# Optimization experiments

Hardware: AMD Instinct MI355X
Metric: run time of the kernel (lower is better)

The kernel has to match this reference:

```python
import jax, jax.numpy as jnp
import numpy as np

B, H, S, D = 4, 16, 2048, 128

def setup_inputs() -> dict:
    key = jax.random.key(0)
    k1, k2 = jax.random.split(key)
    x2 = jax.random.normal(k1, (B, H, S, D), dtype=jnp.float32)
    x3 = jax.random.normal(k2, (B, H, S, D), dtype=jnp.float32)
    return {"x2": x2, "x3": x3}

def reference(x2, x3):
    # scores: [B,H,S,S] = x2 @ x3^T (unscaled)
    scores = jnp.einsum('bhqd,bhkd->bhqk', x2, x3)
    probs = jax.nn.softmax(scores, axis=-1)
    # output: [B,H,S,D] = probs @ x3
    return jnp.einsum('bhqk,bhkd->bhqd', probs, x3)
```

## Files before the change

### kernel.cpp

```cpp
#include <hip/hip_runtime.h>
#include <hip/hip_bf16.h>

typedef __attribute__((ext_vector_type(4))) float f32x4;
typedef _Float16 f16;
typedef __attribute__((ext_vector_type(8))) _Float16 f16x8;
typedef __attribute__((ext_vector_type(2))) __fp16 pk16x2;
typedef __attribute__((ext_vector_type(2))) unsigned int uint2v;

#define S_LEN 2048
#define D_DIM 128
#define QBLK 128
#define KVBLK 64
#define NKV (S_LEN / KVBLK)
#define LOG2E 1.44269504088896340736f
#define EXP2(x) __builtin_amdgcn_exp2f(x)

__device__ __forceinline__ unsigned cvtpk(float a, float b) {
    union { pk16x2 p; unsigned u; } v;
    v.p = __builtin_amdgcn_cvt_pkrtz(a, b);
    return v.u;
}

__device__ __forceinline__ float hired_max(float x) {
    uint2v s = __builtin_amdgcn_permlane16_swap(__float_as_uint(x), __float_as_uint(x), false, false);
    float m = fmaxf(__uint_as_float(s.x), __uint_as_float(s.y));
    uint2v s2 = __builtin_amdgcn_permlane32_swap(__float_as_uint(m), __float_as_uint(m), false, false);
    return fmaxf(__uint_as_float(s2.x), __uint_as_float(s2.y));
}
__device__ __forceinline__ float hired_sum(float x) {
    uint2v s = __builtin_amdgcn_permlane16_swap(__float_as_uint(x), __float_as_uint(x), false, false);
    float m = __uint_as_float(s.x) + __uint_as_float(s.y);
    uint2v s2 = __builtin_amdgcn_permlane32_swap(__float_as_uint(m), __float_as_uint(m), false, false);
    return __uint_as_float(s2.x) + __uint_as_float(s2.y);
}

__global__ __launch_bounds__(256, 2) void attn_kernel(
    const float* __restrict__ Q, const float* __restrict__ KV,
    float* __restrict__ Out)
{
    unsigned b = blockIdx.x;
    unsigned cpx = gridDim.x >> 3;
    unsigned work = (b & 7u) * cpx + (b >> 3);
    unsigned head = work >> 4;
    unsigned qt = work & 15u;

    const float* Qh = Q + (size_t)head * (S_LEN * D_DIM) + (size_t)qt * QBLK * D_DIM;
    const float* Kh = KV + (size_t)head * (S_LEN * D_DIM);
    float* Oh = Out + (size_t)head * (S_LEN * D_DIM) + (size_t)qt * QBLK * D_DIM;

    const int tid = threadIdx.x;
    const int wv = tid >> 6;
    const int lane = tid & 63;
    const int lo = lane & 15;
    const int hi = lane >> 4;

    __shared__ __align__(16) f16 Ksh[KVBLK * D_DIM];
    __shared__ __align__(16) f16 Vsh[D_DIM * KVBLK];

    const int srow = (tid >> 5) * 8;
    const int scol = (tid & 31) * 4;

    f16x8 qf[2][4];
    #pragma unroll
    for (int t = 0; t < 2; ++t) {
        const float* qr = Qh + (wv * 32 + t * 16 + lo) * D_DIM + hi * 8;
        #pragma unroll
        for (int kc = 0; kc < 4; ++kc) {
            f32x4 a = *(const f32x4*)(qr + kc * 32);
            f32x4 c = *(const f32x4*)(qr + kc * 32 + 4);
            union { unsigned u[4]; f16x8 v; } q;
            q.u[0] = cvtpk(a[0] * LOG2E, a[1] * LOG2E);
            q.u[1] = cvtpk(a[2] * LOG2E, a[3] * LOG2E);
            q.u[2] = cvtpk(c[0] * LOG2E, c[1] * LOG2E);
            q.u[3] = cvtpk(c[2] * LOG2E, c[3] * LOG2E);
            qf[t][kc] = q.v;
        }
    }

    f32x4 oacc[2][8];
    #pragma unroll
    for (int t = 0; t < 2; ++t)
        #pragma unroll
        for (int n = 0; n < 8; ++n) oacc[t][n] = (f32x4){0.f, 0.f, 0.f, 0.f};
    float mr[2] = {-1e30f, -1e30f};
    float lr[2] = {0.f, 0.f};

    f32x4 stg[8];
    uint2v kw[8];
    unsigned vw[4][4];

    #define STAGE_LOAD(KT) do {                                               \
        const float* p_ = Kh + (size_t)(KT) * KVBLK * D_DIM + (size_t)srow * D_DIM + scol; \
        _Pragma("unroll")                                                     \
        for (int i_ = 0; i_ < 8; ++i_) stg[i_] = *(const f32x4*)(p_ + i_ * D_DIM); \
    } while (0)

    #define STAGE_PACK() do {                                                 \
        _Pragma("unroll")                                                     \
        for (int i_ = 0; i_ < 8; ++i_) {                                      \
            kw[i_].x = cvtpk(stg[i_][0], stg[i_][1]);                         \
            kw[i_].y = cvtpk(stg[i_][2], stg[i_][3]);                         \
        }                                                                     \
        _Pragma("unroll")                                                     \
        for (int j_ = 0; j_ < 4; ++j_) {                                      \
            vw[j_][0] = cvtpk(stg[0][j_], stg[1][j_]);                        \
            vw[j_][1] = cvtpk(stg[2][j_], stg[3][j_]);                        \
            vw[j_][2] = cvtpk(stg[4][j_], stg[5][j_]);                        \
            vw[j_][3] = cvtpk(stg[6][j_], stg[7][j_]);                        \
        }                                                                     \
    } while (0)

    #define STAGE_WRITE() do {                                                \
        _Pragma("unroll")                                                     \
        for (int i_ = 0; i_ < 8; ++i_) {                                      \
            int row_ = srow + i_;                                             \
            int fK_ = (row_ & 7) ^ ((row_ >> 3) & 7);                         \
            *(uint2v*)&Ksh[row_ * D_DIM + (scol ^ (fK_ << 3))] = kw[i_];      \
        }                                                                     \
        _Pragma("unroll")                                                     \
        for (int j_ = 0; j_ < 4; ++j_) {                                      \
            int d_ = scol + j_;                                               \
            int g_ = (d_ & 7) ^ ((d_ >> 3) & 7);                              \
            union { unsigned u[4]; f16x8 v; } w_;                             \
            w_.u[0] = vw[j_][0]; w_.u[1] = vw[j_][1];                         \
            w_.u[2] = vw[j_][2]; w_.u[3] = vw[j_][3];                         \
            *(f16x8*)&Vsh[d_ * KVBLK + (srow ^ (g_ << 3))] = w_.v;            \
        }                                                                     \
    } while (0)

    STAGE_LOAD(0);
    STAGE_PACK();
    STAGE_WRITE();
    __syncthreads();

    for (int kt = 0; kt < NKV; ++kt) {
        if (kt + 1 < NKV) STAGE_LOAD(kt + 1);

        f32x4 st[2][4];
        #pragma unroll
        for (int t = 0; t < 2; ++t)
            #pragma unroll
            for (int m = 0; m < 4; ++m) st[t][m] = (f32x4){0.f, 0.f, 0.f, 0.f};
        __builtin_amdgcn_s_setprio(1);
        #pragma unroll
        for (int m = 0; m < 4; ++m) {
            int row = m * 16 + lo;
            int fK = (row & 7) ^ ((row >> 3) & 7);
            #pragma unroll
            for (int kc = 0; kc < 4; ++kc) {
                f16x8 kf = *(const f16x8*)&Ksh[row * D_DIM + ((kc * 32 + hi * 8) ^ (fK << 3))];
                st[0][m] = __builtin_amdgcn_mfma_f32_16x16x32_f16(kf, qf[0][kc], st[0][m], 0, 0, 0);
                st[1][m] = __builtin_amdgcn_mfma_f32_16x16x32_f16(kf, qf[1][kc], st[1][m], 0, 0, 0);
            }
        }
        __builtin_amdgcn_s_setprio(0);

        f16x8 pf[2][2];
        #pragma unroll
        for (int t = 0; t < 2; ++t) {
            float mm[4];
            #pragma unroll
            for (int m = 0; m < 4; ++m)
                mm[m] = fmaxf(fmaxf(st[t][m][0], st[t][m][1]),
                              fmaxf(st[t][m][2], st[t][m][3]));
            float tmax = fmaxf(fmaxf(mm[0], mm[1]), fmaxf(mm[2], mm[3]));
            tmax = hired_max(tmax);

            bool skip = __all(tmax - mr[t] <= 11.5415603f);
            float mnew = skip ? mr[t] : fmaxf(mr[t], tmax);

            float sm[4];
            #pragma unroll
            for (int m = 0; m < 4; ++m) {
                float p0 = EXP2(st[t][m][0] - mnew);
                float p1 = EXP2(st[t][m][1] - mnew);
                float p2 = EXP2(st[t][m][2] - mnew);
                float p3 = EXP2(st[t][m][3] - mnew);
                st[t][m][0] = p0; st[t][m][1] = p1;
                st[t][m][2] = p2; st[t][m][3] = p3;
                sm[m] = (p0 + p1) + (p2 + p3);
            }
            float ls = (sm[0] + sm[1]) + (sm[2] + sm[3]);
            ls = hired_sum(ls);

            if (!skip) {
                float scale = EXP2(mr[t] - mnew);
                lr[t] = lr[t] * scale + ls;
                float sc4[4];
                #pragma unroll
                for (int r = 0; r < 4; ++r) sc4[r] = __shfl(scale, hi * 4 + r, 64);
                #pragma unroll
                for (int n = 0; n < 8; ++n)
                    #pragma unroll
                    for (int r = 0; r < 4; ++r) oacc[t][n][r] *= sc4[r];
                mr[t] = mnew;
            } else {
                lr[t] += ls;
            }

            unsigned cc[4][2];
            #pragma unroll
            for (int m = 0; m < 4; ++m) {
                cc[m][0] = cvtpk(st[t][m][0], st[t][m][1]);
                cc[m][1] = cvtpk(st[t][m][2], st[t][m][3]);
            }
            #pragma unroll
            for (int kc2 = 0; kc2 < 2; ++kc2) {
                unsigned r0 = cc[2 * kc2][0], r1 = cc[2 * kc2][1];
                unsigned r2 = cc[2 * kc2 + 1][0], r3 = cc[2 * kc2 + 1][1];
                uint2v s02 = __builtin_amdgcn_permlane32_swap(r0, r2, false, false);
                uint2v s13 = __builtin_amdgcn_permlane32_swap(r1, r3, false, false);
                uint2v t02 = __builtin_amdgcn_permlane16_swap(s02.x, s02.y, false, false);
                uint2v t13 = __builtin_amdgcn_permlane16_swap(s13.x, s13.y, false, false);
                union { unsigned u[4]; f16x8 v; } pu;
                pu.u[0] = t02.x; pu.u[1] = t13.x; pu.u[2] = t02.y; pu.u[3] = t13.y;
                pf[t][kc2] = pu.v;
            }
        }

        __builtin_amdgcn_s_setprio(1);
        #pragma unroll
        for (int kc2 = 0; kc2 < 2; ++kc2) {
            #pragma unroll
            for (int n = 0; n < 8; ++n) {
                int d = n * 16 + lo;
                int g = (d & 7) ^ ((d >> 3) & 7);
                f16x8 vf = *(const f16x8*)&Vsh[d * KVBLK + ((kc2 * 32 + hi * 8) ^ (g << 3))];
                oacc[0][n] = __builtin_amdgcn_mfma_f32_16x16x32_f16(pf[0][kc2], vf, oacc[0][n], 0, 0, 0);
                oacc[1][n] = __builtin_amdgcn_mfma_f32_16x16x32_f16(pf[1][kc2], vf, oacc[1][n], 0, 0, 0);
            }
        }
        __builtin_amdgcn_s_setprio(0);

        if (kt + 1 < NKV) STAGE_PACK();

        __syncthreads();
        if (kt + 1 < NKV) {
            STAGE_WRITE();
            __syncthreads();
        }
    }

    #pragma unroll
    for (int t = 0; t < 2; ++t) {
        float inv = 1.0f / lr[t];
        float rl[4];
        #pragma unroll
        for (int r = 0; r < 4; ++r) rl[r] = __shfl(inv, hi * 4 + r, 64);
        #pragma unroll
        for (int n = 0; n < 8; ++n)
            #pragma unroll
            for (int r = 0; r < 4; ++r)
                Oh[(wv * 32 + t * 16 + hi * 4 + r) * D_DIM + n * 16 + lo] = oacc[t][n][r] * rl[r];
    }
}

extern "C" void kernel_launch(void* const* d_in, const int* in_sizes, int n_in,
                              void* d_out, int out_size, void* d_ws, size_t ws_size,
                              hipStream_t stream) {
    const float* x2 = (const float*)d_in[0];
    const float* x3 = (const float*)d_in[1];
    float* out = (float*)d_out;
    dim3 grid(1024), block(256);
    hipLaunchKernelGGL(attn_kernel, grid, block, 0, stream, x2, x3, out);
}
```

Baseline: 170.6 us.

## Compute softmax row sums via MFMA with ones and fuse staging conversion

The softmax denominator is now accumulated by extra MFMA instructions that multiply the fp16 probability fragments by a ones vector. This replaces the per-tile VALU additions and cross-lane permlane sum reduction. The accumulator lands in the output layout, so the final per-row shuffle of the inverse is dropped. The separate pack stage is removed and fp32-to-fp16 conversion is folded into the LDS write after the barrier, which frees registers but moves conversion work onto the critical path. The max reduction is also rewritten as a flatter fmax tree, and row sums now come from fp16-rounded probabilities.

```diff
diff --git a/kernel.cpp b/kernel.cpp
--- a/kernel.cpp
+++ b/kernel.cpp
@@ -26,12 +26,6 @@
     float m = fmaxf(__uint_as_float(s.x), __uint_as_float(s.y));
     uint2v s2 = __builtin_amdgcn_permlane32_swap(__float_as_uint(m), __float_as_uint(m), false, false);
     return fmaxf(__uint_as_float(s2.x), __uint_as_float(s2.y));
-}
-__device__ __forceinline__ float hired_sum(float x) {
-    uint2v s = __builtin_amdgcn_permlane16_swap(__float_as_uint(x), __float_as_uint(x), false, false);
-    float m = __uint_as_float(s.x) + __uint_as_float(s.y);
-    uint2v s2 = __builtin_amdgcn_permlane32_swap(__float_as_uint(m), __float_as_uint(m), false, false);
-    return __uint_as_float(s2.x) + __uint_as_float(s2.y);
 }
 
 __global__ __launch_bounds__(256, 2) void attn_kernel(
@@ -60,6 +54,11 @@
     const int srow = (tid >> 5) * 8;
     const int scol = (tid & 31) * 4;
 
+    union { unsigned u[4]; f16x8 v; } onesu;
+    onesu.u[0] = 0x3C003C00u; onesu.u[1] = 0x3C003C00u;
+    onesu.u[2] = 0x3C003C00u; onesu.u[3] = 0x3C003C00u;
+    const f16x8 onesf = onesu.v;
+
     f16x8 qf[2][4];
     #pragma unroll
     for (int t = 0; t < 2; ++t) {
@@ -78,16 +77,16 @@
     }
 
     f32x4 oacc[2][8];
+    f32x4 lacc[2];
     #pragma unroll
-    for (int t = 0; t < 2; ++t)
+    for (int t = 0; t < 2; ++t) {
         #pragma unroll
         for (int n = 0; n < 8; ++n) oacc[t][n] = (f32x4){0.f, 0.f, 0.f, 0.f};
+        lacc[t] = (f32x4){0.f, 0.f, 0.f, 0.f};
+    }
     float mr[2] = {-1e30f, -1e30f};
-    float lr[2] = {0.f, 0.f};
 
     f32x4 stg[8];
-    uint2v kw[8];
-    unsigned vw[4][4];
 
     #define STAGE_LOAD(KT) do {                                               \
         const float* p_ = Kh + (size_t)(KT) * KVBLK * D_DIM + (size_t)srow * D_DIM + scol; \
@@ -95,41 +94,30 @@
         for (int i_ = 0; i_ < 8; ++i_) stg[i_] = *(const f32x4*)(p_ + i_ * D_DIM); \
     } while (0)
 
-    #define STAGE_PACK() do {                                                 \
-        _Pragma("unroll")                                                     \
-        for (int i_ = 0; i_ < 8; ++i_) {                                      \
-            kw[i_].x = cvtpk(stg[i_][0], stg[i_][1]);                         \
-            kw[i_].y = cvtpk(stg[i_][2], stg[i_][3]);                         \
-        }                                                                     \
-        _Pragma("unroll")                                                     \
-        for (int j_ = 0; j_ < 4; ++j_) {                                      \
-            vw[j_][0] = cvtpk(stg[0][j_], stg[1][j_]);                        \
-            vw[j_][1] = cvtpk(stg[2][j_], stg[3][j_]);                        \
-            vw[j_][2] = cvtpk(stg[4][j_], stg[5][j_]);                        \
-            vw[j_][3] = cvtpk(stg[6][j_], stg[7][j_]);                        \
-        }                                                                     \
-    } while (0)
-
     #define STAGE_WRITE() do {                                                \
         _Pragma("unroll")                                                     \
         for (int i_ = 0; i_ < 8; ++i_) {                                      \
             int row_ = srow + i_;                                             \
             int fK_ = (row_ & 7) ^ ((row_ >> 3) & 7);                         \
-            *(uint2v*)&Ksh[row_ * D_DIM + (scol ^ (fK_ << 3))] = kw[i_];      \
+            uint2v w_;                                                        \
+            w_.x = cvtpk(stg[i_][0], stg[i_][1]);                             \
+            w_.y = cvtpk(stg[i_][2], stg[i_][3]);                             \
+            *(uint2v*)&Ksh[row_ * D_DIM + (scol ^ (fK_ << 3))] = w_;          \
         }                                                                     \
         _Pragma("unroll")                                                     \
         for (int j_ = 0; j_ < 4; ++j_) {                                      \
             int d_ = scol + j_;                                               \
             int g_ = (d_ & 7) ^ ((d_ >> 3) & 7);                              \
             union { unsigned u[4]; f16x8 v; } w_;                             \
-            w_.u[0] = vw[j_][0]; w_.u[1] = vw[j_][1];                         \
-            w_.u[2] = vw[j_][2]; w_.u[3] = vw[j_][3];                         \
+            w_.u[0] = cvtpk(stg[0][j_], stg[1][j_]);                          \
+            w_.u[1] = cvtpk(stg[2][j_], stg[3][j_]);                          \
+            w_.u[2] = cvtpk(stg[4][j_], stg[5][j_]);                          \
+            w_.u[3] = cvtpk(stg[6][j_], stg[7][j_]);                          \
             *(f16x8*)&Vsh[d_ * KVBLK + (srow ^ (g_ << 3))] = w_.v;            \
         }                                                                     \
     } while (0)
 
     STAGE_LOAD(0);
-    STAGE_PACK();
     STAGE_WRITE();
     __syncthreads();
 
@@ -158,34 +146,28 @@
         f16x8 pf[2][2];
         #pragma unroll
         for (int t = 0; t < 2; ++t) {
-            float mm[4];
-            #pragma unroll
-            for (int m = 0; m < 4; ++m)
-                mm[m] = fmaxf(fmaxf(st[t][m][0], st[t][m][1]),
-                              fmaxf(st[t][m][2], st[t][m][3]));
-            float tmax = fmaxf(fmaxf(mm[0], mm[1]), fmaxf(mm[2], mm[3]));
-            tmax = hired_max(tmax);
+            float a0 = fmaxf(fmaxf(st[t][0][0], st[t][0][1]), st[t][0][2]);
+            float a1 = fmaxf(fmaxf(st[t][0][3], st[t][1][0]), st[t][1][1]);
+            float a2 = fmaxf(fmaxf(st[t][1][2], st[t][1][3]), st[t][2][0]);
+            float a3 = fmaxf(fmaxf(st[t][2][1], st[t][2][2]), st[t][2][3]);
+            float a4 = fmaxf(fmaxf(st[t][3][0], st[t][3][1]), st[t][3][2]);
+            float b0 = fmaxf(fmaxf(a0, a1), a2);
+            float b1 = fmaxf(fmaxf(a3, a4), st[t][3][3]);
+            float tmax = hired_max(fmaxf(b0, b1));
 
             bool skip = __all(tmax - mr[t] <= 11.5415603f);
             float mnew = skip ? mr[t] : fmaxf(mr[t], tmax);
 
-            float sm[4];
             #pragma unroll
             for (int m = 0; m < 4; ++m) {
-                float p0 = EXP2(st[t][m][0] - mnew);
-                float p1 = EXP2(st[t][m][1] - mnew);
-                float p2 = EXP2(st[t][m][2] - mnew);
-                float p3 = EXP2(st[t][m][3] - mnew);
-                st[t][m][0] = p0; st[t][m][1] = p1;
-                st[t][m][2] = p2; st[t][m][3] = p3;
-                sm[m] = (p0 + p1) + (p2 + p3);
-            }
-            float ls = (sm[0] + sm[1]) + (sm[2] + sm[3]);
-            ls = hired_sum(ls);
+                st[t][m][0] = EXP2(st[t][m][0] - mnew);
+                st[t][m][1] = EXP2(st[t][m][1] - mnew);
+                st[t][m][2] = EXP2(st[t][m][2] - mnew);
+                st[t][m][3] = EXP2(st[t][m][3] - mnew);
+            }
 
             if (!skip) {
                 float scale = EXP2(mr[t] - mnew);
-                lr[t] = lr[t] * scale + ls;
                 float sc4[4];
                 #pragma unroll
                 for (int r = 0; r < 4; ++r) sc4[r] = __shfl(scale, hi * 4 + r, 64);
@@ -193,9 +175,9 @@
                 for (int n = 0; n < 8; ++n)
                     #pragma unroll
                     for (int r = 0; r < 4; ++r) oacc[t][n][r] *= sc4[r];
+                #pragma unroll
+                for (int r = 0; r < 4; ++r) lacc[t][r] *= sc4[r];
                 mr[t] = mnew;
-            } else {
-                lr[t] += ls;
             }
 
             unsigned cc[4][2];
@@ -221,6 +203,8 @@
         __builtin_amdgcn_s_setprio(1);
         #pragma unroll
         for (int kc2 = 0; kc2 < 2; ++kc2) {
+            lacc[0] = __builtin_amdgcn_mfma_f32_16x16x32_f16(pf[0][kc2], onesf, lacc[0], 0, 0, 0);
+            lacc[1] = __builtin_amdgcn_mfma_f32_16x16x32_f16(pf[1][kc2], onesf, lacc[1], 0, 0, 0);
             #pragma unroll
             for (int n = 0; n < 8; ++n) {
                 int d = n * 16 + lo;
@@ -232,8 +216,6 @@
         }
         __builtin_amdgcn_s_setprio(0);
 
-        if (kt + 1 < NKV) STAGE_PACK();
-
         __syncthreads();
         if (kt + 1 < NKV) {
             STAGE_WRITE();
@@ -243,10 +225,9 @@
 
     #pragma unroll
     for (int t = 0; t < 2; ++t) {
-        float inv = 1.0f / lr[t];
         float rl[4];
         #pragma unroll
-        for (int r = 0; r < 4; ++r) rl[r] = __shfl(inv, hi * 4 + r, 64);
+        for (int r = 0; r < 4; ++r) rl[r] = 1.0f / lacc[t][r];
         #pragma unroll
         for (int n = 0; n < 8; ++n)
             #pragma unroll
```

Result: faster. 162.8 us, median of 2 (-4.6%).
